# Optimization experiments

Hardware: AMD Instinct MI355X
Metric: run time of the kernel (lower is better)

Reference implementation:

```python
import jax, jax.numpy as jnp
import numpy as np

NH, DH, BS, HS = 8, 16, 8, 3           # heads, head dim, block size, halo size
WIN = BS + 2 * HS                      # 14
DIM, DIM_V = 256, 256
SCALE = DH ** -0.5


def setup_inputs() -> dict:
    key = jax.random.key(0)
    k1, k2, k3, k4, k5 = jax.random.split(key, 5)
    x = jax.random.normal(k1, (8, DIM, 64, 64), jnp.float32)
    q_w = jax.random.normal(k2, (NH * DH, DIM), jnp.float32) * (DIM ** -0.5)
    kv_w = jax.random.normal(k3, (NH * DH + DIM_V, DIM), jnp.float32) * (DIM ** -0.5)
    height_rel = jax.random.normal(k4, (2 * WIN - 1, DH), jnp.float32) * SCALE
    width_rel = jax.random.normal(k5, (2 * WIN - 1, DH), jnp.float32) * SCALE
    return {"x": x, "q_w": q_w, "kv_w": kv_w, "height_rel": height_rel, "width_rel": width_rel}


def _rel_logits_1d(q, rel_k, perm):
    N, Hq, Wq, d = q.shape
    rel_size = rel_k.shape[0]
    win = (rel_size + 1) // 2
    x = jnp.einsum('nhwd,rd->nhwr', q, rel_k).reshape(N * Hq, Wq, rel_size)
    x = jnp.pad(x, ((0, 0), (0, 0), (0, 1))).reshape(N * Hq, Wq * (rel_size + 1))
    x = jnp.pad(x, ((0, 0), (0, rel_size - Wq))).reshape(N * Hq, Wq + 1, rel_size)
    x = x[:, :Wq, win - 1:]
    x = jnp.broadcast_to(x.reshape(N, Hq, 1, Wq, win), (N, Hq, win, Wq, win))
    return x.transpose(perm)


def _pos_embed(q, height_rel, width_rel):
    Bh, nb, HW, dh = q.shape
    qb = q.reshape(-1, BS, BS, dh)
    rw = _rel_logits_1d(qb, width_rel, (0, 1, 3, 2, 4))
    rh = _rel_logits_1d(qb.transpose(0, 2, 1, 3), height_rel, (0, 3, 1, 4, 2))
    return (rh + rw).reshape(Bh, nb, HW, -1)


def reference(x, q_w, kv_w, height_rel, width_rel):
    B, C, H, W = x.shape
    nHb, nWb = H // BS, W // BS
    nb = nHb * nWb
    dvh = DIM_V // NH

    # q: 1x1 conv + block-unfold -> (B*nh, nb, bs*bs, dh)
    q = jnp.einsum('bchw,oc->bohw', x, q_w)
    q = q.reshape(B, NH, DH, nHb, BS, nWb, BS).transpose(0, 1, 3, 5, 4, 6, 2)
    q = q.reshape(B * NH, nb, BS * BS, DH)

    kv = jnp.einsum('bchw,oc->bohw', x, kv_w)
    kvp = jnp.pad(kv, ((0, 0), (0, 0), (HS, HS), (HS, HS)))
    rows = jnp.arange(nHb)[:, None] * BS + jnp.arange(WIN)[None, :]
    cols = jnp.arange(nWb)[:, None] * BS + jnp.arange(WIN)[None, :]
    wins = kvp[:, :, rows][:, :, :, :, cols]
    wins = wins.transpose(0, 1, 2, 4, 3, 5)
    wins = wins.reshape(B, NH, DH + dvh, nb, WIN * WIN).transpose(0, 1, 3, 4, 2)
    wins = wins.reshape(B * NH, nb, WIN * WIN, DH + dvh)
    k, v = wins[..., :DH], wins[..., DH:]

    attn = jnp.einsum('znqd,znkd->znqk', q, k) * SCALE + _pos_embed(q, height_rel, width_rel)
    attn = jax.nn.softmax(attn, axis=-1)
    out = jnp.einsum('znqk,znkd->znqd', attn, v)        # (B*nh, nb, bs*bs, dvh)

    # fold blocks back to (B, dim_v, H, W)
    out = out.reshape(B, NH, nHb, nWb, BS, BS, dvh).transpose(0, 1, 6, 2, 4, 3, 5)
    return out.reshape(B, DIM_V, H, W)
```

## Files before the change

### kernel.cpp

```cpp
#include <hip/hip_runtime.h>
#include <hip/hip_bf16.h>

#define LOG2E 1.4426950408889634f

typedef __attribute__((ext_vector_type(8))) short bf16x8;
typedef __attribute__((ext_vector_type(4))) float f32x4;
typedef __attribute__((ext_vector_type(16))) float f32x16;

__device__ __forceinline__ short f2bf(float a) {
  __hip_bfloat16 h = __float2bfloat16(a);
  return *reinterpret_cast<short*>(&h);
}
__device__ __forceinline__ unsigned pkbf(float a, float b) {
  return (unsigned)(unsigned short)f2bf(a) | ((unsigned)(unsigned short)f2bf(b) << 16);
}
__device__ __forceinline__ unsigned cvtpk(float a, float b) {
  unsigned r;
  asm("v_cvt_pk_bf16_f32 %0, %1, %2" : "=v"(r) : "v"(a), "v"(b));
  return r;
}
__device__ __forceinline__ float bfu2f(unsigned u16v) {
  unsigned v = u16v << 16; float f; __builtin_memcpy(&f, &v, 4); return f;
}
union FragU8 { unsigned d[4]; bf16x8 v; };
union KU { uint4 u; bf16x8 v; };

__global__ __launch_bounds__(256) void haloattn_cvt(
    const float* __restrict__ x, const float* __restrict__ q_w,
    const float* __restrict__ kv_w, unsigned short* __restrict__ xT,
    unsigned short* __restrict__ w_bf, unsigned short* __restrict__ vpln)
{
  __shared__ float Ld[64][68];
  const int t = threadIdx.x;
  const int pt = blockIdx.x, kt = blockIdx.y, b = blockIdx.z;
  const int flat = ((b << 2) + kt) * 64 + pt;
  {
    const int idx = flat * 64 + (t & 63);
    if (t < 64) {
      const float wv = (idx < 32768) ? q_w[idx] : kv_w[idx - 32768];
      w_bf[idx] = (unsigned short)f2bf(wv);
    }
  }
  {
    unsigned short* pl = vpln + (size_t)flat * 5040;
    for (int e = t; e < 944; e += 256) {
      int off;
      if (e < 216) {
        off = e;
      } else if (e < 432) {
        off = 4824 + (e - 216);
      } else {
        const int tt = e - 432;
        const int y = 3 + (tt >> 3);
        const int cidx = tt & 7;
        off = y * 72 + (cidx < 3 ? cidx : cidx + 64);
      }
      pl[off] = 0;
    }
  }
  const float* xb = x + ((size_t)b * 256 + (kt << 6)) * 4096 + (pt << 6);
#pragma unroll
  for (int ps = 0; ps < 4; ++ps) {
    const int kloc = (ps << 4) + (t >> 4);
    const int ploc = (t & 15) << 2;
    float4 v = *(const float4*)(xb + (size_t)kloc * 4096 + ploc);
    *(float4*)&Ld[kloc][ploc] = v;
  }
  __syncthreads();
  const int pl = t >> 2;
  const int ks = (t & 3) << 4;
  float f[16];
#pragma unroll
  for (int i = 0; i < 16; ++i) f[i] = Ld[ks + i][pl];
  uint4 o0, o1;
  o0.x = pkbf(f[0], f[1]);   o0.y = pkbf(f[2], f[3]);
  o0.z = pkbf(f[4], f[5]);   o0.w = pkbf(f[6], f[7]);
  o1.x = pkbf(f[8], f[9]);   o1.y = pkbf(f[10], f[11]);
  o1.z = pkbf(f[12], f[13]); o1.w = pkbf(f[14], f[15]);
  unsigned short* op = xT + ((size_t)(b << 12) + (pt << 6) + pl) * 256 + (kt << 6) + ks;
  *(uint4*)op = o0;
  *(uint4*)(op + 8) = o1;
}

__global__ __launch_bounds__(512, 4) void haloattn_proj_mfma(
    const unsigned short* __restrict__ xT, const unsigned short* __restrict__ w_bf,
    unsigned short* __restrict__ q_bf, unsigned short* __restrict__ kbuf,
    unsigned short* __restrict__ vpln)
{
  __shared__ unsigned short Wt[256][68];
  __shared__ unsigned short Xt[128][68];
  const int tid = threadIdx.x;
  const int w = tid >> 6, l = tid & 63;
  const int b = blockIdx.z, oBase = blockIdx.y << 8, pBase = blockIdx.x << 7;
  const int wm = w >> 1, wn = w & 1;
  const int g = l >> 4, c = l & 15;

  f32x4 acc[4][4] = {};

  const int srow = tid >> 3;
  const int se3  = (tid & 7) << 3;

  for (int chk = 0; chk < 4; ++chk) {
    const int k0 = chk << 6;
#pragma unroll
    for (int ps = 0; ps < 4; ++ps) {
      const int row = (ps << 6) + srow;
      uint4 wv = *(const uint4*)(w_bf + (size_t)(oBase + row) * 256 + k0 + se3);
      char* dst = (char*)&Wt[0][0] + row * 136 + (se3 << 1);
      *(uint2*)dst = make_uint2(wv.x, wv.y);
      *(uint2*)(dst + 8) = make_uint2(wv.z, wv.w);
    }
#pragma unroll
    for (int ps = 0; ps < 2; ++ps) {
      const int p = (ps << 6) + srow;
      uint4 xv = *(const uint4*)(xT + ((size_t)(b << 12) + pBase + p) * 256 + k0 + se3);
      char* dst = (char*)&Xt[0][0] + p * 136 + (se3 << 1);
      *(uint2*)dst = make_uint2(xv.x, xv.y);
      *(uint2*)(dst + 8) = make_uint2(xv.z, xv.w);
    }
    __syncthreads();
#pragma unroll
    for (int kk = 0; kk < 2; ++kk) {
      FragU8 bfr[4];
#pragma unroll
      for (int nf = 0; nf < 4; ++nf) {
        const char* src = (const char*)&Xt[0][0]
            + ((wn << 6) + (nf << 4) + c) * 136 + (kk << 6) + (g << 4);
        uint2 lo = *(const uint2*)src, hi2 = *(const uint2*)(src + 8);
        bfr[nf].d[0] = lo.x; bfr[nf].d[1] = lo.y;
        bfr[nf].d[2] = hi2.x; bfr[nf].d[3] = hi2.y;
      }
#pragma unroll
      for (int mf = 0; mf < 4; ++mf) {
        const char* src = (const char*)&Wt[0][0]
            + ((wm << 6) + (mf << 4) + c) * 136 + (kk << 6) + (g << 4);
        uint2 lo = *(const uint2*)src, hi2 = *(const uint2*)(src + 8);
        FragU8 af;
        af.d[0] = lo.x; af.d[1] = lo.y; af.d[2] = hi2.x; af.d[3] = hi2.y;
#pragma unroll
        for (int nf = 0; nf < 4; ++nf)
          acc[mf][nf] = __builtin_amdgcn_mfma_f32_16x16x32_bf16(af.v, bfr[nf].v, acc[mf][nf], 0, 0, 0);
      }
    }
    __syncthreads();
  }
#pragma unroll
  for (int mf = 0; mf < 4; ++mf) {
    const int o = oBase + (wm << 6) + (mf << 4) + (g << 2);
#pragma unroll
    for (int nf = 0; nf < 4; ++nf) {
      const int p = pBase + (wn << 6) + (nf << 4) + c;
      if (o < 128) {
        uint2 pk2 = make_uint2(pkbf(acc[mf][nf][0], acc[mf][nf][1]),
                               pkbf(acc[mf][nf][2], acc[mf][nf][3]));
        const int head = o >> 4;
        const int z = (b << 3) + head;
        const int y = p >> 6, xx = p & 63;
        const int nbb = ((y >> 3) << 3) + (xx >> 3);
        const int qi = ((y & 7) << 3) + (xx & 7);
        *(uint2*)(q_bf + (((size_t)z * 64 + nbb) * 64 + qi) * 16 + (o & 15)) = pk2;
      } else {
        const int ch = o - 128;
        const int head = (ch * 1366) >> 16;
        const int wi = ch - head * 48;
        const int b8h = (b << 3) + head;
        if (wi < 16) {
          uint2 pk2 = make_uint2(pkbf(acc[mf][nf][0], acc[mf][nf][1]),
                                 pkbf(acc[mf][nf][2], acc[mf][nf][3]));
          *(uint2*)(kbuf + ((size_t)b8h * 4096 + p) * 16 + wi) = pk2;
        } else {
          const int d = wi - 16;
          const int y = p >> 6, xx = p & 63;
          unsigned short* vp = vpln + (size_t)(b8h * 32 + d) * 5040
                               + (size_t)(y + 3) * 72 + (xx + 3);
          vp[0]     = (unsigned short)f2bf(acc[mf][nf][0]);
          vp[5040]  = (unsigned short)f2bf(acc[mf][nf][1]);
          vp[10080] = (unsigned short)f2bf(acc[mf][nf][2]);
          vp[15120] = (unsigned short)f2bf(acc[mf][nf][3]);
        }
      }
    }
  }
}

__global__ __launch_bounds__(128, 2) void haloattn_attn_direct(
    const unsigned short* __restrict__ q_bf, const unsigned short* __restrict__ kbuf,
    const unsigned short* __restrict__ vpln,
    const float* __restrict__ height_rel, const float* __restrict__ width_rel,
    float* __restrict__ out)
{
  __shared__ __align__(16) unsigned short SM[5376];

  const int tid = threadIdx.x;
  const int w = tid >> 6;
  const int l = tid & 63;
  const int q32 = l & 31, hi = l >> 5;
  const int wg = blockIdx.x;
  const int swz = ((wg & 7) << 9) | (wg >> 3);
  const int z = swz >> 6;
  const int nb = swz & 63;
  const int b = z >> 3, head = z & 7;
  const int bi = nb >> 3, bj = nb & 7;
  const int swapA = (l ^ 32) << 2;
  const f32x16 z16 = {};
  const float qs = 0.25f * LOG2E;

  const unsigned short* qtile = q_bf + ((size_t)z * 64 + nb) * 1024;
  bf16x8 qfrag[2];
  qfrag[0] = *(const bf16x8*)(qtile + q32 * 16 + 8 * hi);
  qfrag[1] = *(const bf16x8*)(qtile + (32 + q32) * 16 + 8 * hi);

  unsigned short* HRs = SM;
  unsigned short* WRs = SM + 768;
  if (tid < 54) {
    const int u = tid >> 1, d0 = (tid & 1) << 3;
    float4 a = *(const float4*)(height_rel + u * 16 + d0);
    float4 b4 = *(const float4*)(height_rel + u * 16 + d0 + 4);
    uint4 o;
    o.x = cvtpk(a.x * LOG2E, a.y * LOG2E);
    o.y = cvtpk(a.z * LOG2E, a.w * LOG2E);
    o.z = cvtpk(b4.x * LOG2E, b4.y * LOG2E);
    o.w = cvtpk(b4.z * LOG2E, b4.w * LOG2E);
    *(uint4*)(HRs + u * 24 + d0) = o;
    a = *(const float4*)(width_rel + u * 16 + d0);
    b4 = *(const float4*)(width_rel + u * 16 + d0 + 4);
    o.x = cvtpk(a.x * LOG2E, a.y * LOG2E);
    o.y = cvtpk(a.z * LOG2E, a.w * LOG2E);
    o.z = cvtpk(b4.x * LOG2E, b4.y * LOG2E);
    o.w = cvtpk(b4.z * LOG2E, b4.w * LOG2E);
    *(uint4*)(WRs + u * 24 + d0) = o;
  } else if (tid < 64) {
    const int t = tid - 54;
    const int u = 27 + (t >> 1), d0 = (t & 1) << 3;
    uint4 o = {};
    *(uint4*)(HRs + u * 24 + d0) = o;
    *(uint4*)(WRs + u * 24 + d0) = o;
  }
  __syncthreads();

  {
    bf16x8 hfr = *(const bf16x8*)((const char*)HRs + q32 * 48 + 16 * hi);
    bf16x8 wfr = *(const bf16x8*)((const char*)WRs + q32 * 48 + 16 * hi);
    f32x16 h0 = __builtin_amdgcn_mfma_f32_32x32x16_bf16(hfr, qfrag[0], z16, 0, 0, 0);
    f32x16 h1 = __builtin_amdgcn_mfma_f32_32x32x16_bf16(hfr, qfrag[1], z16, 0, 0, 0);
    f32x16 w0 = __builtin_amdgcn_mfma_f32_32x32x16_bf16(wfr, qfrag[0], z16, 0, 0, 0);
    f32x16 w1 = __builtin_amdgcn_mfma_f32_32x32x16_bf16(wfr, qfrag[1], z16, 0, 0, 0);
    __syncthreads();
    if (w == 0) {
#pragma unroll
      for (int r = 0; r < 16; ++r) {
        const int u = (r & 3) + 8 * (r >> 2) + 4 * hi;
        if (u >= 6 && u < 27) {
          const int rr = u - 6;
          SM[rr * 64 + q32]               = (unsigned short)f2bf(h0[r]);
          SM[(21 + rr) * 64 + q32]        = (unsigned short)f2bf(h1[r]);
          SM[2688 + rr * 64 + q32]        = (unsigned short)f2bf(w0[r]);
          SM[2688 + (21 + rr) * 64 + q32] = (unsigned short)f2bf(w1[r]);
        }
      }
    }
  }
  __syncthreads();

  const int qw = q32 & 7;
  float wreg[2][8];
#pragma unroll
  for (int nt = 0; nt < 2; ++nt)
#pragma unroll
    for (int t = 0; t < 8; ++t) {
      const int jt = (t < 4 ? t : t + 4) + 4 * hi;
      if (jt < 14)
        wreg[nt][t] = bfu2f(SM[2688 + (nt * 21 + 7 - qw + jt) * 64 + q32]);
      else
        wreg[nt][t] = -1e30f;
    }

  const int qh0 = q32 >> 3;
  const unsigned short* Hp0 = SM + (7 - qh0) * 64 + q32;
  const unsigned short* Hp1 = SM + (24 - qh0) * 64 + q32;

  const int jj = q32 & 15, ir = q32 >> 4;
  const int xx = bj * 8 + jj - 3;
  const bool jok = (jj < 14) && ((unsigned)xx < 64u);
  const unsigned short* kb = kbuf + ((size_t)((b << 3) + head) * 4096 + xx) * 16 + 8 * hi;
  const int yy0 = bi * 8 + ir - 3;
  const unsigned short* vb = vpln + (size_t)(((b << 3) + head) * 32 + q32) * 5040
                             + (bi * 8) * 72 + bj * 8 + 8 * hi;

  const int c0w = w ? 4 : 0;
  const int ncw = w ? 3 : 4;

  f32x16 acc[2] = {};
  float lrow[2] = {0.f, 0.f};

  KU k4; k4.u = make_uint4(0, 0, 0, 0);
  {
    const int yy = yy0 + 2 * c0w;
    if (jok && (unsigned)yy < 64u) k4.u = *(const uint4*)(kb + (size_t)yy * 1024);
  }
  bf16x8 v0n = *(const bf16x8*)(vb + (2 * c0w) * 72);
  bf16x8 v1n = *(const bf16x8*)(vb + (2 * c0w + 1) * 72);

  for (int ci = 0; ci < ncw; ++ci) {
    const int c = c0w + ci;
    const bf16x8 kf = k4.v;
    const bf16x8 vf0 = v0n, vf1 = v1n;
    if (ci < ncw - 1) {
      const int yy = yy0 + 2 * (c + 1);
      KU kn; kn.u = make_uint4(0, 0, 0, 0);
      if (jok && (unsigned)yy < 64u) kn.u = *(const uint4*)(kb + (size_t)yy * 1024);
      k4 = kn;
      v0n = *(const bf16x8*)(vb + (2 * c + 2) * 72);
      v1n = *(const bf16x8*)(vb + (2 * c + 3) * 72);
    }
#pragma unroll
    for (int nt = 0; nt < 2; ++nt) {
      f32x16 Cs = __builtin_amdgcn_mfma_f32_32x32x16_bf16(kf, qfrag[nt], z16, 0, 0, 0);
      const unsigned short* Hp = nt ? Hp1 : Hp0;
      const float hA = bfu2f(Hp[(2 * c) * 64]);
      const float hB = bfu2f(Hp[(2 * c + 1) * 64]);
      float p[16];
#pragma unroll
      for (int r = 0; r < 16; ++r) {
        const float wv = wreg[nt][(r & 3) + 4 * ((r >> 2) & 1)];
        const float h = (r < 8) ? hA : hB;
        p[r] = exp2f(fmaf(Cs[r], qs, h + wv));
      }
      {
        float s0 = (p[0] + p[1]) + (p[2] + p[3]);
        float s1 = (p[4] + p[5]) + (p[6] + p[7]);
        float s2 = (p[8] + p[9]) + (p[10] + p[11]);
        float s3 = (p[12] + p[13]) + (p[14] + p[15]);
        lrow[nt] += (s0 + s1) + (s2 + s3);
      }
      unsigned dw[8], xw[8];
#pragma unroll
      for (int k = 0; k < 8; ++k) dw[k] = cvtpk(p[2 * k], p[2 * k + 1]);
#pragma unroll
      for (int k = 0; k < 8; ++k)
        xw[k] = (unsigned)__builtin_amdgcn_ds_bpermute(swapA, (int)dw[k]);
      FragU8 f0, f1;
      f0.d[0] = hi ? xw[2] : dw[0];
      f0.d[1] = hi ? xw[3] : dw[1];
      f0.d[2] = hi ? dw[2] : xw[0];
      f0.d[3] = hi ? dw[3] : xw[1];
      f1.d[0] = hi ? xw[6] : dw[4];
      f1.d[1] = hi ? xw[7] : dw[5];
      f1.d[2] = hi ? dw[6] : xw[4];
      f1.d[3] = hi ? dw[7] : xw[5];
      acc[nt] = __builtin_amdgcn_mfma_f32_32x32x16_bf16(vf0, f0.v, acc[nt], 0, 0, 0);
      acc[nt] = __builtin_amdgcn_mfma_f32_32x32x16_bf16(vf1, f1.v, acc[nt], 0, 0, 0);
    }
  }

  __syncthreads();
  float* F = (float*)SM;
  if (w == 0) {
#pragma unroll
    for (int r = 0; r < 16; ++r) F[l * 17 + r] = acc[1][r];
    F[l * 17 + 16] = lrow[1];
  } else {
#pragma unroll
    for (int r = 0; r < 16; ++r) F[1088 + l * 17 + r] = acc[0][r];
    F[1088 + l * 17 + 16] = lrow[0];
  }
  __syncthreads();
  const int nt = w;
  float am[16];
  float lm;
  if (w == 0) {
#pragma unroll
    for (int r = 0; r < 16; ++r) am[r] = acc[0][r] + F[1088 + l * 17 + r];
    lm = lrow[0] + F[1088 + l * 17 + 16];
  } else {
#pragma unroll
    for (int r = 0; r < 16; ++r) am[r] = acc[1][r] + F[l * 17 + r];
    lm = lrow[1] + F[l * 17 + 16];
  }
  const float L = lm + __shfl_xor(lm, 32);
  const float invL = 1.f / L;
  const int qt = nt * 32 + q32;
  const int yq = bi * 8 + (qt >> 3);
  const int xq = bj * 8 + (q32 & 7);
  float* obase = out + ((size_t)(b * 256 + head * 32) * 4096) + yq * 64 + xq;
#pragma unroll
  for (int r = 0; r < 16; ++r) {
    const int d = (r & 3) + 8 * (r >> 2) + 4 * hi;
    obase[(size_t)d * 4096] = am[r] * invL;
  }
}

extern "C" void kernel_launch(void* const* d_in, const int* in_sizes, int n_in,
                              void* d_out, int out_size, void* d_ws, size_t ws_size,
                              hipStream_t stream) {
  const float* x          = (const float*)d_in[0];
  const float* q_w        = (const float*)d_in[1];
  const float* kv_w       = (const float*)d_in[2];
  const float* height_rel = (const float*)d_in[3];
  const float* width_rel  = (const float*)d_in[4];
  float* out = (float*)d_out;

  unsigned short* q_bf = (unsigned short*)d_ws;
  unsigned short* xT   = q_bf + (size_t)4194304;
  unsigned short* w_bf = xT + (size_t)8388608;
  unsigned short* kbuf = w_bf + (size_t)131072;
  unsigned short* vpln = kbuf + (size_t)4194304;

  haloattn_cvt<<<dim3(64, 4, 8), 256, 0, stream>>>(x, q_w, kv_w, xT, w_bf, vpln);
  haloattn_proj_mfma<<<dim3(32, 2, 8), 512, 0, stream>>>(xT, w_bf, q_bf, kbuf, vpln);
  haloattn_attn_direct<<<4096, 128, 0, stream>>>(q_bf, kbuf, vpln,
                                                 height_rel, width_rel, out);
}
```

Before: 72.09 us.

## Fuse fp32-to-bf16 conversion into projection GEMM and swizzle workgroups

The separate conversion kernel that transposed x to bf16 and converted the weights is removed. The projection kernel now reads fp32 x and the weights directly and converts them in registers; the X tile is gathered straight from global memory into MFMA fragments without going through LDS. A small kernel still zeroes the halo padding of the V planes, and the grid is flattened with a swizzled block index meant to improve L2 locality. This drops the xT/w_bf workspace round-trip, but the X loads are now strided 4-byte accesses spread over eight rows per lane, and each x element is reloaded by both output-half workgroups.

```diff
diff --git a/kernel.cpp b/kernel.cpp
--- a/kernel.cpp
+++ b/kernel.cpp
@@ -25,73 +25,41 @@
 union FragU8 { unsigned d[4]; bf16x8 v; };
 union KU { uint4 u; bf16x8 v; };
 
-__global__ __launch_bounds__(256) void haloattn_cvt(
+__global__ __launch_bounds__(256) void haloattn_prep(
+    unsigned short* __restrict__ vpln)
+{
+  unsigned short* pl = vpln + (size_t)blockIdx.x * 5040;
+  for (int e = threadIdx.x; e < 944; e += 256) {
+    int off;
+    if (e < 216) {
+      off = e;
+    } else if (e < 432) {
+      off = 4824 + (e - 216);
+    } else {
+      const int tt = e - 432;
+      const int y = 3 + (tt >> 3);
+      const int cidx = tt & 7;
+      off = y * 72 + (cidx < 3 ? cidx : cidx + 64);
+    }
+    pl[off] = 0;
+  }
+}
+
+__global__ __launch_bounds__(512, 4) void haloattn_proj_mfma(
     const float* __restrict__ x, const float* __restrict__ q_w,
-    const float* __restrict__ kv_w, unsigned short* __restrict__ xT,
-    unsigned short* __restrict__ w_bf, unsigned short* __restrict__ vpln)
-{
-  __shared__ float Ld[64][68];
-  const int t = threadIdx.x;
-  const int pt = blockIdx.x, kt = blockIdx.y, b = blockIdx.z;
-  const int flat = ((b << 2) + kt) * 64 + pt;
-  {
-    const int idx = flat * 64 + (t & 63);
-    if (t < 64) {
-      const float wv = (idx < 32768) ? q_w[idx] : kv_w[idx - 32768];
-      w_bf[idx] = (unsigned short)f2bf(wv);
-    }
-  }
-  {
-    unsigned short* pl = vpln + (size_t)flat * 5040;
-    for (int e = t; e < 944; e += 256) {
-      int off;
-      if (e < 216) {
-        off = e;
-      } else if (e < 432) {
-        off = 4824 + (e - 216);
-      } else {
-        const int tt = e - 432;
-        const int y = 3 + (tt >> 3);
-        const int cidx = tt & 7;
-        off = y * 72 + (cidx < 3 ? cidx : cidx + 64);
-      }
-      pl[off] = 0;
-    }
-  }
-  const float* xb = x + ((size_t)b * 256 + (kt << 6)) * 4096 + (pt << 6);
-#pragma unroll
-  for (int ps = 0; ps < 4; ++ps) {
-    const int kloc = (ps << 4) + (t >> 4);
-    const int ploc = (t & 15) << 2;
-    float4 v = *(const float4*)(xb + (size_t)kloc * 4096 + ploc);
-    *(float4*)&Ld[kloc][ploc] = v;
-  }
-  __syncthreads();
-  const int pl = t >> 2;
-  const int ks = (t & 3) << 4;
-  float f[16];
-#pragma unroll
-  for (int i = 0; i < 16; ++i) f[i] = Ld[ks + i][pl];
-  uint4 o0, o1;
-  o0.x = pkbf(f[0], f[1]);   o0.y = pkbf(f[2], f[3]);
-  o0.z = pkbf(f[4], f[5]);   o0.w = pkbf(f[6], f[7]);
-  o1.x = pkbf(f[8], f[9]);   o1.y = pkbf(f[10], f[11]);
-  o1.z = pkbf(f[12], f[13]); o1.w = pkbf(f[14], f[15]);
-  unsigned short* op = xT + ((size_t)(b << 12) + (pt << 6) + pl) * 256 + (kt << 6) + ks;
-  *(uint4*)op = o0;
-  *(uint4*)(op + 8) = o1;
-}
-
-__global__ __launch_bounds__(512, 4) void haloattn_proj_mfma(
-    const unsigned short* __restrict__ xT, const unsigned short* __restrict__ w_bf,
+    const float* __restrict__ kv_w,
     unsigned short* __restrict__ q_bf, unsigned short* __restrict__ kbuf,
     unsigned short* __restrict__ vpln)
 {
   __shared__ unsigned short Wt[256][68];
-  __shared__ unsigned short Xt[128][68];
   const int tid = threadIdx.x;
   const int w = tid >> 6, l = tid & 63;
-  const int b = blockIdx.z, oBase = blockIdx.y << 8, pBase = blockIdx.x << 7;
+  const int wg = blockIdx.x;
+  const int swz = ((wg & 7) << 6) | (wg >> 3);
+  const int oSel = swz & 1;
+  const int px   = (swz >> 1) & 31;
+  const int b    = swz >> 6;
+  const int oBase = oSel << 8, pBase = px << 7;
   const int wm = w >> 1, wn = w & 1;
   const int g = l >> 4, c = l & 15;
 
@@ -100,35 +68,43 @@
   const int srow = tid >> 3;
   const int se3  = (tid & 7) << 3;
 
+  const float* xb = x + (size_t)b * (256 * 4096);
+
   for (int chk = 0; chk < 4; ++chk) {
     const int k0 = chk << 6;
 #pragma unroll
     for (int ps = 0; ps < 4; ++ps) {
       const int row = (ps << 6) + srow;
-      uint4 wv = *(const uint4*)(w_bf + (size_t)(oBase + row) * 256 + k0 + se3);
+      const int o = oBase + row;
+      const float* wr = (o < 128 ? q_w + (size_t)o * 256
+                                 : kv_w + (size_t)(o - 128) * 256) + k0 + se3;
+      float4 a = *(const float4*)wr;
+      float4 b4 = *(const float4*)(wr + 4);
       char* dst = (char*)&Wt[0][0] + row * 136 + (se3 << 1);
-      *(uint2*)dst = make_uint2(wv.x, wv.y);
-      *(uint2*)(dst + 8) = make_uint2(wv.z, wv.w);
-    }
-#pragma unroll
-    for (int ps = 0; ps < 2; ++ps) {
-      const int p = (ps << 6) + srow;
-      uint4 xv = *(const uint4*)(xT + ((size_t)(b << 12) + pBase + p) * 256 + k0 + se3);
-      char* dst = (char*)&Xt[0][0] + p * 136 + (se3 << 1);
-      *(uint2*)dst = make_uint2(xv.x, xv.y);
-      *(uint2*)(dst + 8) = make_uint2(xv.z, xv.w);
+      *(uint2*)dst = make_uint2(cvtpk(a.x, a.y), cvtpk(a.z, a.w));
+      *(uint2*)(dst + 8) = make_uint2(cvtpk(b4.x, b4.y), cvtpk(b4.z, b4.w));
     }
     __syncthreads();
 #pragma unroll
     for (int kk = 0; kk < 2; ++kk) {
       FragU8 bfr[4];
+      const float* xg = xb + (size_t)(k0 + (kk << 5) + (g << 3)) * 4096
+                        + pBase + (wn << 6) + c;
 #pragma unroll
       for (int nf = 0; nf < 4; ++nf) {
-        const char* src = (const char*)&Xt[0][0]
-            + ((wn << 6) + (nf << 4) + c) * 136 + (kk << 6) + (g << 4);
-        uint2 lo = *(const uint2*)src, hi2 = *(const uint2*)(src + 8);
-        bfr[nf].d[0] = lo.x; bfr[nf].d[1] = lo.y;
-        bfr[nf].d[2] = hi2.x; bfr[nf].d[3] = hi2.y;
+        const float* xp = xg + (nf << 4);
+        float f0 = xp[0];
+        float f1 = xp[4096];
+        float f2 = xp[2 * 4096];
+        float f3 = xp[3 * 4096];
+        float f4 = xp[4 * 4096];
+        float f5 = xp[5 * 4096];
+        float f6 = xp[6 * 4096];
+        float f7 = xp[7 * 4096];
+        bfr[nf].d[0] = cvtpk(f0, f1);
+        bfr[nf].d[1] = cvtpk(f2, f3);
+        bfr[nf].d[2] = cvtpk(f4, f5);
+        bfr[nf].d[3] = cvtpk(f6, f7);
       }
 #pragma unroll
       for (int mf = 0; mf < 4; ++mf) {
@@ -401,13 +377,11 @@
   float* out = (float*)d_out;
 
   unsigned short* q_bf = (unsigned short*)d_ws;
-  unsigned short* xT   = q_bf + (size_t)4194304;
-  unsigned short* w_bf = xT + (size_t)8388608;
-  unsigned short* kbuf = w_bf + (size_t)131072;
+  unsigned short* kbuf = q_bf + (size_t)4194304;
   unsigned short* vpln = kbuf + (size_t)4194304;
 
-  haloattn_cvt<<<dim3(64, 4, 8), 256, 0, stream>>>(x, q_w, kv_w, xT, w_bf, vpln);
-  haloattn_proj_mfma<<<dim3(32, 2, 8), 512, 0, stream>>>(xT, w_bf, q_bf, kbuf, vpln);
+  haloattn_prep<<<2048, 256, 0, stream>>>(vpln);
+  haloattn_proj_mfma<<<512, 512, 0, stream>>>(x, q_w, kv_w, q_bf, kbuf, vpln);
   haloattn_attn_direct<<<4096, 128, 0, stream>>>(q_bf, kbuf, vpln,
                                                  height_rel, width_rel, out);
 }
```

Measured after the change: 79.09 us. 9.7% more time.
